# Performance work log

Measured on AMD Instinct MI355X. Metric: run time of the kernel, lower is better.

Reference implementation:

```python
import jax, jax.numpy as jnp
import numpy as np

B, S, E = 2, 2048, 1024
H, D = 16, 64  # num_heads, head_dim


def setup_inputs() -> dict:
    key = jax.random.key(0)
    k1, k2, k3 = jax.random.split(key, 3)
    x = jax.random.normal(k1, (B, S, E), dtype=jnp.float32)
    # nnx normal() init has stddev 0.01; scale to keep magnitudes realistic
    w_qkv = jax.random.normal(k2, (E, H, 3 * D), dtype=jnp.float32) * 0.01
    w_out = jax.random.normal(k3, (H, D, E), dtype=jnp.float32) * 0.01
    return {"x": x, "w_qkv": w_qkv, "w_out": w_out}


def _attention(q, k, v):
    # q,k,v: [B, S, H, D]
    dtype = q.dtype
    logits = jnp.einsum('bqhd,bkhd->bhqk', q.astype(jnp.float32), k.astype(jnp.float32))
    logits = logits / jnp.sqrt(jnp.float32(q.shape[-1]))
    mask = jnp.tril(jnp.ones((q.shape[1], q.shape[1]), dtype=jnp.bool_))
    neg = jnp.asarray(-0.7 * jnp.finfo(logits.dtype).max, dtype=logits.dtype)
    logits = jnp.where(mask, logits, neg)
    probs = jax.nn.softmax(logits, axis=-1).astype(dtype)
    return jnp.einsum('bhqk,bkhd->bqhd', probs, v)


def reference(x, w_qkv, w_out):
    # qkv projection: [B,S,E] x [E,H,3D] -> [B,S,H,3D]
    qkv = jnp.einsum('bse,ehd->bshd', x, w_qkv)
    q, k, v = jnp.split(qkv, 3, axis=-1)
    out = _attention(q, k, v)  # [B,S,H,D]
    # output projection contracts (H,D) -> E
    return jnp.einsum('bshd,hde->bse', out, w_out)
```

## Files before the change

### kernel.cpp

```cpp
#include <hip/hip_runtime.h>

typedef unsigned short u16;
typedef unsigned int u32;
typedef __attribute__((ext_vector_type(8))) short bf16x8;
typedef __attribute__((ext_vector_type(4))) float f32x4;
typedef __attribute__((ext_vector_type(16))) float f32x16;
typedef __attribute__((ext_vector_type(4))) u32 u32x4;

#define MFMA16(a, b, c) __builtin_amdgcn_mfma_f32_16x16x32_bf16((a), (b), (c), 0, 0, 0)
#define MFMA32(a, b, c) __builtin_amdgcn_mfma_f32_32x32x16_bf16((a), (b), (c), 0, 0, 0)

__device__ __forceinline__ void async_lds16(void* lds, const void* g) {
  __builtin_amdgcn_global_load_lds(
      (const __attribute__((address_space(1))) void*)g,
      (__attribute__((address_space(3))) void*)lds, 16, 0, 0);
}

__device__ __forceinline__ u16 f2bf(float f) {
  union { float f; unsigned u; } v; v.f = f;
  unsigned r = v.u + 0x7fffu + ((v.u >> 16) & 1u);
  return (u16)(r >> 16);
}

__device__ __forceinline__ u32 cvt_pk_bf16(float lo, float hi) {
  u32 r;
  asm("v_cvt_pk_bf16_f32 %0, %1, %2" : "=v"(r) : "v"(lo), "v"(hi));
  return r;
}

__device__ __forceinline__ float exp2_fast(float x) {
  float r;
  asm("v_exp_f32 %0, %1" : "=v"(r) : "v"(x));
  return r;
}

__device__ __forceinline__ void pswap(u32& a, u32& b) {
  asm("v_permlane32_swap_b32 %0, %1" : "+v"(a), "+v"(b));
}


__global__ __launch_bounds__(256) void k_cvt(const float* __restrict__ in, u16* __restrict__ out, int n) {
  int i = (blockIdx.x * 256 + threadIdx.x) * 4;
  if (i >= n) return;
  float4 v = *(const float4*)(in + i);
  ushort4 o;
  o.x = f2bf(v.x); o.y = f2bf(v.y); o.z = f2bf(v.z); o.w = f2bf(v.w);
  *(ushort4*)(out + i) = o;
}

__global__ __launch_bounds__(256) void k_transpose_cvt(const float* __restrict__ in, u16* __restrict__ out,
                                                       int R, int C) {
  __shared__ float tile[32][33];
  int c0 = blockIdx.x * 32, r0 = blockIdx.y * 32;
  int tx = threadIdx.x & 31, ty = threadIdx.x >> 5;
#pragma unroll
  for (int i = 0; i < 32; i += 8)
    tile[ty + i][tx] = in[(long)(r0 + ty + i) * C + c0 + tx];
  __syncthreads();
#pragma unroll
  for (int i = 0; i < 32; i += 8)
    out[(long)(c0 + ty + i) * R + r0 + tx] = f2bf(tile[tx][ty + i]);
}

__global__ __launch_bounds__(256) void k_transpose_v(const u16* __restrict__ V, u16* __restrict__ Vt) {
  int bh = blockIdx.z;
  int s0 = blockIdx.x * 32, d0 = blockIdx.y * 32;
  __shared__ u16 tile[32][33];
  int tx = threadIdx.x & 31, ty = threadIdx.x >> 5;
  const u16* Vb = V + (long)bh * 2048 * 64;
  u16* Vtb = Vt + (long)bh * 64 * 2048;
#pragma unroll
  for (int i = 0; i < 32; i += 8)
    tile[ty + i][tx] = Vb[(long)(s0 + ty + i) * 64 + d0 + tx];
  __syncthreads();
#pragma unroll
  for (int i = 0; i < 32; i += 8)
    Vtb[(long)(d0 + ty + i) * 2048 + s0 + tx] = tile[tx][ty + i];
}


template <int BM, int BN, int NW, int WN, int MR, int NR>
__device__ __forceinline__ void gemm_core_pipe(const u16* __restrict__ A, const u16* __restrict__ Bt,
                                               int K, long row0, long col0,
                                               u16* sA, u16* sB, f32x4 (&acc)[MR][NR]) {
  const int NTHR = NW * 64;
  const int ABYTES = BM * 64 * 2;
  const int BBYTES = BN * 64 * 2;
  const int t = threadIdx.x;
  const int lane = t & 63, g = lane >> 4, m16 = lane & 15;
  const int wid = t >> 6, wr = wid / WN, wc = wid % WN;
  const int nkt = K >> 6;

  auto stage = [&](int buf, int kt) {
    const int k0 = kt << 6;
#pragma unroll
    for (int it = 0; it < ABYTES / (NTHR * 16); ++it) {
      int i = it * NTHR + t;
      int r = i >> 3, c = i & 7, cs = c ^ (r & 7);
      async_lds16((char*)sA + buf * ABYTES + i * 16, A + (row0 + r) * K + k0 + cs * 8);
    }
#pragma unroll
    for (int it = 0; it < BBYTES / (NTHR * 16); ++it) {
      int i = it * NTHR + t;
      int r = i >> 3, c = i & 7, cs = c ^ (r & 7);
      async_lds16((char*)sB + buf * BBYTES + i * 16, Bt + (col0 + r) * K + k0 + cs * 8);
    }
  };

  stage(0, 0);
  stage(1, 1);
  int cur = 0;
  for (int kt = 0; kt < nkt; ++kt) {
    if (kt + 1 < nkt) asm volatile("s_waitcnt vmcnt(8)" ::: "memory");
    else              asm volatile("s_waitcnt vmcnt(0)" ::: "memory");
    __builtin_amdgcn_s_barrier();
    __builtin_amdgcn_sched_barrier(0);
    const char* bA = (const char*)sA + cur * ABYTES;
    const char* bB = (const char*)sB + cur * BBYTES;
#pragma unroll
    for (int kk6 = 0; kk6 < 2; ++kk6) {
      const int ke = kk6 * 32 + 8 * g;
      bf16x8 av[MR], bv[NR];
#pragma unroll
      for (int mi = 0; mi < MR; ++mi) {
        int row = wr * (MR * 16) + mi * 16 + m16;
        av[mi] = *(const bf16x8*)(bA + (row << 7) + ((ke << 1) ^ ((row & 7) << 4)));
      }
#pragma unroll
      for (int ni = 0; ni < NR; ++ni) {
        int row = wc * (NR * 16) + ni * 16 + m16;
        bv[ni] = *(const bf16x8*)(bB + (row << 7) + ((ke << 1) ^ ((row & 7) << 4)));
      }
#pragma unroll
      for (int mi = 0; mi < MR; ++mi)
#pragma unroll
        for (int ni = 0; ni < NR; ++ni)
          acc[mi][ni] = MFMA16(av[mi], bv[ni], acc[mi][ni]);
    }
    __builtin_amdgcn_sched_barrier(0);
    __builtin_amdgcn_s_barrier();
    if (kt + 2 < nkt) stage(cur, kt + 2);
    cur ^= 1;
  }
}

__global__ __launch_bounds__(512, 2) void k_gemm_qkv(const u16* __restrict__ xb, const u16* __restrict__ wT,
                                                     u16* __restrict__ Qo, u16* __restrict__ Ko,
                                                     u16* __restrict__ Vo) {
  __shared__ __align__(16) u16 sA[2 * 256 * 64];
  __shared__ __align__(16) u16 sB[2 * 256 * 64];
  f32x4 acc[8][4];
  const f32x4 z = {0.f, 0.f, 0.f, 0.f};
#pragma unroll
  for (int mi = 0; mi < 8; ++mi)
#pragma unroll
    for (int ni = 0; ni < 4; ++ni) acc[mi][ni] = z;
  const int L = blockIdx.x;
  const int xcd = L & 7, idx = L >> 3;
  const int rowt = xcd * 2 + (idx & 1);
  const int colt = idx >> 1;
  long row0 = (long)rowt * 256, col0 = (long)colt * 256;
  gemm_core_pipe<256, 256, 8, 4, 8, 4>(xb, wT, 1024, row0, col0, sA, sB, acc);
  const int t = threadIdx.x;
  const int lane = t & 63, g = lane >> 4, m16 = lane & 15;
  const int wid = t >> 6, wr = wid >> 2, wc = wid & 3;
#pragma unroll
  for (int mi = 0; mi < 8; ++mi) {
#pragma unroll
    for (int ni = 0; ni < 4; ++ni) {
      int col = (int)col0 + wc * 64 + ni * 16 + m16;
      int h = col / 192, rem = col - h * 192;
      int which = rem >> 6, d = rem & 63;
#pragma unroll
      for (int r = 0; r < 4; ++r) {
        int row = (int)row0 + wr * 128 + mi * 16 + 4 * g + r;
        int b = row >> 11, s = row & 2047;
        long off = (((long)(b * 16 + h)) * 2048 + s) * 64 + d;
        float v = acc[mi][ni][r];
        if (which == 0) Qo[off] = f2bf(v * 0.18033688f);
        else if (which == 1) Ko[off] = f2bf(v);
        else Vo[off] = f2bf(v);
      }
    }
  }
}

__global__ __launch_bounds__(256) void k_gemm_out(const u16* __restrict__ Ob, const u16* __restrict__ wT,
                                                  float* __restrict__ out) {
  __shared__ __align__(16) u16 sA[2 * 128 * 64];
  __shared__ __align__(16) u16 sB[2 * 128 * 64];
  f32x4 acc[4][4];
  const f32x4 z = {0.f, 0.f, 0.f, 0.f};
#pragma unroll
  for (int mi = 0; mi < 4; ++mi)
#pragma unroll
    for (int ni = 0; ni < 4; ++ni) acc[mi][ni] = z;
  const int L = blockIdx.x;
  const int xcd = L & 7, idx = L >> 3;
  const int rowt = xcd * 4 + (idx & 3);
  const int colt = idx >> 2;
  long row0 = (long)rowt * 128, col0 = (long)colt * 128;
  gemm_core_pipe<128, 128, 4, 2, 4, 4>(Ob, wT, 1024, row0, col0, sA, sB, acc);
  const int t = threadIdx.x;
  const int lane = t & 63, g = lane >> 4, m16 = lane & 15;
  const int wid = t >> 6, wr = wid >> 1, wc = wid & 1;
#pragma unroll
  for (int mi = 0; mi < 4; ++mi) {
#pragma unroll
    for (int ni = 0; ni < 4; ++ni) {
#pragma unroll
      for (int r = 0; r < 4; ++r) {
        long row = row0 + wr * 64 + mi * 16 + 4 * g + r;
        long col = col0 + wc * 64 + ni * 16 + m16;
        out[row * 1024 + col] = acc[mi][ni][r];
      }
    }
  }
}


template <bool DIAG>
__device__ __forceinline__ void attn_sub(const char* Kt, const char* Vt, int bsub,
                                         bf16x8 qf0, bf16x8 qf1, bf16x8 qf2, bf16x8 qf3,
                                         f32x16& acc0, f32x16& acc1, float& l,
                                         int q5, int hi) {
  const int x7 = q5 & 7;
  const int rowK = (bsub * 32 + q5) << 7;
  bf16x8 k0 = *(const bf16x8*)(Kt + rowK + (((0 + hi) ^ x7) << 4));
  bf16x8 k1 = *(const bf16x8*)(Kt + rowK + (((2 + hi) ^ x7) << 4));
  bf16x8 k2 = *(const bf16x8*)(Kt + rowK + (((4 + hi) ^ x7) << 4));
  bf16x8 k3 = *(const bf16x8*)(Kt + rowK + (((6 + hi) ^ x7) << 4));
  const int rowV0 = q5 << 7, rowV1 = (q5 + 32) << 7;
  bf16x8 v00 = *(const bf16x8*)(Vt + rowV0 + (((bsub * 4 + 0 + hi) ^ x7) << 4));
  bf16x8 v01 = *(const bf16x8*)(Vt + rowV1 + (((bsub * 4 + 0 + hi) ^ x7) << 4));
  bf16x8 v10 = *(const bf16x8*)(Vt + rowV0 + (((bsub * 4 + 2 + hi) ^ x7) << 4));
  bf16x8 v11 = *(const bf16x8*)(Vt + rowV1 + (((bsub * 4 + 2 + hi) ^ x7) << 4));

  f32x16 s;
#pragma unroll
  for (int r = 0; r < 16; ++r) s[r] = 0.f;
  s = MFMA32(k0, qf0, s);
  s = MFMA32(k1, qf1, s);
  s = MFMA32(k2, qf2, s);
  s = MFMA32(k3, qf3, s);

  float p[16];
#pragma unroll
  for (int r = 0; r < 16; ++r) {
    float pv = exp2_fast(s[r]);
    if (DIAG) {
      int crow = (r & 3) + 8 * (r >> 2) + 4 * hi;
      pv = (crow <= q5) ? pv : 0.f;
    }
    p[r] = pv;
  }
  l += (((p[0] + p[1]) + (p[2] + p[3])) + ((p[4] + p[5]) + (p[6] + p[7]))) +
       (((p[8] + p[9]) + (p[10] + p[11])) + ((p[12] + p[13]) + (p[14] + p[15])));

  u32 a0 = cvt_pk_bf16(p[0], p[1]), a1 = cvt_pk_bf16(p[2], p[3]);
  u32 b0 = cvt_pk_bf16(p[4], p[5]), b1 = cvt_pk_bf16(p[6], p[7]);
  pswap(a0, b0); pswap(a1, b1);
  u32 c0 = cvt_pk_bf16(p[8], p[9]), c1 = cvt_pk_bf16(p[10], p[11]);
  u32 d0 = cvt_pk_bf16(p[12], p[13]), d1 = cvt_pk_bf16(p[14], p[15]);
  pswap(c0, d0); pswap(c1, d1);
  u32x4 t0; t0[0] = a0; t0[1] = a1; t0[2] = b0; t0[3] = b1;
  u32x4 t1; t1[0] = c0; t1[1] = c1; t1[2] = d0; t1[3] = d1;
  bf16x8 pa0 = __builtin_bit_cast(bf16x8, t0);
  bf16x8 pa1 = __builtin_bit_cast(bf16x8, t1);

  acc0 = MFMA32(pa0, v00, acc0);
  acc1 = MFMA32(pa0, v01, acc1);
  acc0 = MFMA32(pa1, v10, acc0);
  acc1 = MFMA32(pa1, v11, acc1);
}

__global__ __launch_bounds__(256) void k_attn(const u16* __restrict__ Qg, const u16* __restrict__ Kg,
                                              const u16* __restrict__ Vtg, u16* __restrict__ Og) {
  __shared__ __align__(16) u16 sK[2][64 * 64];
  __shared__ __align__(16) u16 sV[2][64 * 64];
  const int t = threadIdx.x;
  const int lane = t & 63, q5 = lane & 31, hi = lane >> 5, w = t >> 6;
  const int L = blockIdx.x;
  const int bh = L & 31, q16 = L >> 5;
  const int qt = (q16 < 8) ? q16 : (23 - q16);
  const int b = bh >> 4, h = bh & 15;
  const u16* Qh = Qg + (long)bh * 131072;
  const u16* Kh = Kg + (long)bh * 131072;
  const u16* Vh = Vtg + (long)bh * 131072;
  char* sKb = (char*)sK;
  char* sVb = (char*)sV;

  const int strip = qt * 4 + w;
  const int q0w = strip * 32;
  const int nkt = 2 * qt + 2;

  const u16* Qp = Qh + (long)(q0w + q5) * 64 + hi * 8;
  bf16x8 qf0 = *(const bf16x8*)(Qp);
  bf16x8 qf1 = *(const bf16x8*)(Qp + 16);
  bf16x8 qf2 = *(const bf16x8*)(Qp + 32);
  bf16x8 qf3 = *(const bf16x8*)(Qp + 48);

  f32x16 acc0, acc1;
#pragma unroll
  for (int r = 0; r < 16; ++r) { acc0[r] = 0.f; acc1[r] = 0.f; }
  float l = 0.f;

  auto stage = [&](int buf, int kt) {
    const int kbase = kt << 6;
#pragma unroll
    for (int ps = 0; ps < 2; ++ps) {
      int i = ps * 256 + t;
      int r = i >> 3, c = i & 7, cs = c ^ (r & 7);
      async_lds16(sKb + buf * 8192 + i * 16, Kh + (long)(kbase + r) * 64 + cs * 8);
    }
#pragma unroll
    for (int ps = 0; ps < 2; ++ps) {
      int i = ps * 256 + t;
      int d = i >> 3, c = i & 7, cs = c ^ (d & 7);
      async_lds16(sVb + buf * 8192 + i * 16, Vh + (long)d * 2048 + kbase + cs * 8);
    }
  };

  stage(0, 0);
  int cur = 0;
  for (int kt = 0; kt < nkt; ++kt) {
    __syncthreads();
    if (kt + 1 < nkt) stage(cur ^ 1, kt + 1);
    const char* Kt = sKb + cur * 8192;
    const char* Vt = sVb + cur * 8192;
    const int c2 = 2 * kt;
    if (c2 <= strip) {
      if (c2 == strip) attn_sub<true>(Kt, Vt, 0, qf0, qf1, qf2, qf3, acc0, acc1, l, q5, hi);
      else             attn_sub<false>(Kt, Vt, 0, qf0, qf1, qf2, qf3, acc0, acc1, l, q5, hi);
    }
    if (c2 + 1 <= strip) {
      if (c2 + 1 == strip) attn_sub<true>(Kt, Vt, 1, qf0, qf1, qf2, qf3, acc0, acc1, l, q5, hi);
      else                 attn_sub<false>(Kt, Vt, 1, qf0, qf1, qf2, qf3, acc0, acc1, l, q5, hi);
    }
    cur ^= 1;
  }

  l += __shfl_xor(l, 32);
  float linv = 1.0f / l;
  const long orow_base = (long)b * 2048;
#pragma unroll
  for (int r = 0; r < 16; ++r) {
    int crow = (r & 3) + 8 * (r >> 2) + 4 * hi;
    float lf = __shfl(linv, crow);
    long orow = orow_base + q0w + crow;
    Og[orow * 1024 + h * 64 + q5] = f2bf(acc0[r] * lf);
    Og[orow * 1024 + h * 64 + 32 + q5] = f2bf(acc1[r] * lf);
  }
}


extern "C" void kernel_launch(void* const* d_in, const int* in_sizes, int n_in,
                              void* d_out, int out_size, void* d_ws, size_t ws_size,
                              hipStream_t stream) {
  const float* x = (const float*)d_in[0];
  const float* w_qkv = (const float*)d_in[1];
  const float* w_out = (const float*)d_in[2];
  float* out = (float*)d_out;
  char* ws = (char*)d_ws;

  u16* xb    = (u16*)(ws + 0);
  u16* wqkvT = (u16*)(ws + 8388608L);
  u16* woutT = (u16*)(ws + 14680064L);
  u16* Qb    = (u16*)(ws + 16777216L);
  u16* Kb    = (u16*)(ws + 25165824L);
  u16* Vb    = (u16*)(ws + 33554432L);
  u16* Vt    = (u16*)(ws + 41943040L);
  u16* Ob    = xb;

  k_cvt<<<4096, 256, 0, stream>>>(x, xb, 4194304);
  k_transpose_cvt<<<dim3(96, 32), 256, 0, stream>>>(w_qkv, wqkvT, 1024, 3072);
  k_transpose_cvt<<<dim3(32, 32), 256, 0, stream>>>(w_out, woutT, 1024, 1024);
  k_gemm_qkv<<<dim3(192), 512, 0, stream>>>(xb, wqkvT, Qb, Kb, Vb);
  k_transpose_v<<<dim3(64, 2, 32), 256, 0, stream>>>(Vb, Vt);
  k_attn<<<dim3(512), 256, 0, stream>>>(Qb, Kb, Vt, Ob);
  k_gemm_out<<<dim3(256), 256, 0, stream>>>(Ob, woutT, out);
}
```

Measured before the change: 124.7 us.

## Pair low and high causal query tiles per block and deepen K/V prefetch

Each attention block now handles two query tiles (qt and 15-qt) that share one streamed K/V pass, so causal work per block is balanced and K/V tiles loaded for the high tile are reused by the low tile. The grid is halved to 256 blocks. The K/V pipeline now keeps two tiles in flight using explicit vmcnt waits and raw s_barriers instead of __syncthreads with a single-ahead prefetch. This doubles accumulator and Q-fragment registers, which may lower occupancy, and leaves fewer blocks than a full wave across CUs.

```diff
diff --git a/kernel.cpp b/kernel.cpp
--- a/kernel.cpp
+++ b/kernel.cpp
@@ -281,8 +281,8 @@
   const int t = threadIdx.x;
   const int lane = t & 63, q5 = lane & 31, hi = lane >> 5, w = t >> 6;
   const int L = blockIdx.x;
-  const int bh = L & 31, q16 = L >> 5;
-  const int qt = (q16 < 8) ? q16 : (23 - q16);
+  const int bh = L & 31, pr = L >> 5;
+  const int qtA = pr, qtB = 15 - pr;
   const int b = bh >> 4, h = bh & 15;
   const u16* Qh = Qg + (long)bh * 131072;
   const u16* Kh = Kg + (long)bh * 131072;
@@ -290,20 +290,25 @@
   char* sKb = (char*)sK;
   char* sVb = (char*)sV;
 
-  const int strip = qt * 4 + w;
-  const int q0w = strip * 32;
-  const int nkt = 2 * qt + 2;
-
-  const u16* Qp = Qh + (long)(q0w + q5) * 64 + hi * 8;
-  bf16x8 qf0 = *(const bf16x8*)(Qp);
-  bf16x8 qf1 = *(const bf16x8*)(Qp + 16);
-  bf16x8 qf2 = *(const bf16x8*)(Qp + 32);
-  bf16x8 qf3 = *(const bf16x8*)(Qp + 48);
-
-  f32x16 acc0, acc1;
-#pragma unroll
-  for (int r = 0; r < 16; ++r) { acc0[r] = 0.f; acc1[r] = 0.f; }
-  float l = 0.f;
+  const int sL_ = qtA * 4 + w, sH_ = qtB * 4 + w;
+  const int q0L = sL_ * 32, q0H = sH_ * 32;
+  const int nkt = 2 * qtB + 2;
+
+  const u16* QpL = Qh + (long)(q0L + q5) * 64 + hi * 8;
+  bf16x8 qfL0 = *(const bf16x8*)(QpL);
+  bf16x8 qfL1 = *(const bf16x8*)(QpL + 16);
+  bf16x8 qfL2 = *(const bf16x8*)(QpL + 32);
+  bf16x8 qfL3 = *(const bf16x8*)(QpL + 48);
+  const u16* QpH = Qh + (long)(q0H + q5) * 64 + hi * 8;
+  bf16x8 qfH0 = *(const bf16x8*)(QpH);
+  bf16x8 qfH1 = *(const bf16x8*)(QpH + 16);
+  bf16x8 qfH2 = *(const bf16x8*)(QpH + 32);
+  bf16x8 qfH3 = *(const bf16x8*)(QpH + 48);
+
+  f32x16 aL0, aL1, aH0, aH1;
+#pragma unroll
+  for (int r = 0; r < 16; ++r) { aL0[r] = 0.f; aL1[r] = 0.f; aH0[r] = 0.f; aH1[r] = 0.f; }
+  float lL = 0.f, lH = 0.f;
 
   auto stage = [&](int buf, int kt) {
     const int kbase = kt << 6;
@@ -322,34 +327,59 @@
   };
 
   stage(0, 0);
+  stage(1, 1);
   int cur = 0;
+#pragma unroll 1
   for (int kt = 0; kt < nkt; ++kt) {
-    __syncthreads();
-    if (kt + 1 < nkt) stage(cur ^ 1, kt + 1);
+    if (kt + 1 < nkt) asm volatile("s_waitcnt vmcnt(4)" ::: "memory");
+    else              asm volatile("s_waitcnt vmcnt(0)" ::: "memory");
+    __builtin_amdgcn_s_barrier();
+    __builtin_amdgcn_sched_barrier(0);
     const char* Kt = sKb + cur * 8192;
     const char* Vt = sVb + cur * 8192;
     const int c2 = 2 * kt;
-    if (c2 <= strip) {
-      if (c2 == strip) attn_sub<true>(Kt, Vt, 0, qf0, qf1, qf2, qf3, acc0, acc1, l, q5, hi);
-      else             attn_sub<false>(Kt, Vt, 0, qf0, qf1, qf2, qf3, acc0, acc1, l, q5, hi);
-    }
-    if (c2 + 1 <= strip) {
-      if (c2 + 1 == strip) attn_sub<true>(Kt, Vt, 1, qf0, qf1, qf2, qf3, acc0, acc1, l, q5, hi);
-      else                 attn_sub<false>(Kt, Vt, 1, qf0, qf1, qf2, qf3, acc0, acc1, l, q5, hi);
-    }
+    if (c2 <= sH_) {
+      if (c2 == sH_) attn_sub<true>(Kt, Vt, 0, qfH0, qfH1, qfH2, qfH3, aH0, aH1, lH, q5, hi);
+      else           attn_sub<false>(Kt, Vt, 0, qfH0, qfH1, qfH2, qfH3, aH0, aH1, lH, q5, hi);
+    }
+    if (c2 + 1 <= sH_) {
+      if (c2 + 1 == sH_) attn_sub<true>(Kt, Vt, 1, qfH0, qfH1, qfH2, qfH3, aH0, aH1, lH, q5, hi);
+      else               attn_sub<false>(Kt, Vt, 1, qfH0, qfH1, qfH2, qfH3, aH0, aH1, lH, q5, hi);
+    }
+    if (c2 <= sL_) {
+      if (c2 == sL_) attn_sub<true>(Kt, Vt, 0, qfL0, qfL1, qfL2, qfL3, aL0, aL1, lL, q5, hi);
+      else           attn_sub<false>(Kt, Vt, 0, qfL0, qfL1, qfL2, qfL3, aL0, aL1, lL, q5, hi);
+    }
+    if (c2 + 1 <= sL_) {
+      if (c2 + 1 == sL_) attn_sub<true>(Kt, Vt, 1, qfL0, qfL1, qfL2, qfL3, aL0, aL1, lL, q5, hi);
+      else               attn_sub<false>(Kt, Vt, 1, qfL0, qfL1, qfL2, qfL3, aL0, aL1, lL, q5, hi);
+    }
+    __builtin_amdgcn_sched_barrier(0);
+    __builtin_amdgcn_s_barrier();
+    if (kt + 2 < nkt) stage(cur, kt + 2);
     cur ^= 1;
   }
 
-  l += __shfl_xor(l, 32);
-  float linv = 1.0f / l;
   const long orow_base = (long)b * 2048;
+  lH += __shfl_xor(lH, 32);
+  float liH = 1.0f / lH;
 #pragma unroll
   for (int r = 0; r < 16; ++r) {
     int crow = (r & 3) + 8 * (r >> 2) + 4 * hi;
-    float lf = __shfl(linv, crow);
-    long orow = orow_base + q0w + crow;
-    Og[orow * 1024 + h * 64 + q5] = f2bf(acc0[r] * lf);
-    Og[orow * 1024 + h * 64 + 32 + q5] = f2bf(acc1[r] * lf);
+    float lf = __shfl(liH, crow);
+    long orow = orow_base + q0H + crow;
+    Og[orow * 1024 + h * 64 + q5] = f2bf(aH0[r] * lf);
+    Og[orow * 1024 + h * 64 + 32 + q5] = f2bf(aH1[r] * lf);
+  }
+  lL += __shfl_xor(lL, 32);
+  float liL = 1.0f / lL;
+#pragma unroll
+  for (int r = 0; r < 16; ++r) {
+    int crow = (r & 3) + 8 * (r >> 2) + 4 * hi;
+    float lf = __shfl(liL, crow);
+    long orow = orow_base + q0L + crow;
+    Og[orow * 1024 + h * 64 + q5] = f2bf(aL0[r] * lf);
+    Og[orow * 1024 + h * 64 + 32 + q5] = f2bf(aL1[r] * lf);
   }
 }
 
@@ -377,6 +407,6 @@
   k_transpose_cvt<<<dim3(32, 32), 256, 0, stream>>>(w_out, woutT, 1024, 1024);
   k_gemm_qkv<<<dim3(192), 512, 0, stream>>>(xb, wqkvT, Qb, Kb, Vb);
   k_transpose_v<<<dim3(64, 2, 32), 256, 0, stream>>>(Vb, Vt);
-  k_attn<<<dim3(512), 256, 0, stream>>>(Qb, Kb, Vt, Ob);
+  k_attn<<<dim3(256), 256, 0, stream>>>(Qb, Kb, Vt, Ob);
   k_gemm_out<<<dim3(256), 256, 0, stream>>>(Ob, woutT, out);
 }
```

New measurement: 122.5 us. Within noise of the previous version (-1.8%).
